# Kernel tuning notes

Hardware: AMD Instinct MI355X
Metric: run time of the kernel (lower is better)

Reference implementation:

```python
import jax, jax.numpy as jnp
import numpy as np

# Stickbreaking attention (IBM ModuleFormer style) as in the torch module:
#   logits = q @ k^T / sqrt(head_dim)  (causal)
#   z = sigmoid(logits), log_beta = logsigmoid(-logits), both causally masked
#   re_cum_log_beta = einsum('bhij,jk->bhik', log_beta, tril(ones(S,S)))
#     -> re[i,k] = sum_{k <= j <= i} log_beta[i, j]   (full tril incl. diagonal,
#        exactly as written in the source: cum_weight = torch.tril(torch.ones(L,L)))
#   weights = z * exp(re_cum_log_beta);  out = weights @ v
# Note: the torch code applies the causal mask by adding -inf; the only finite,
# NaN-free expression of that math (matching ModuleFormer's masked_fill) is to
# zero out masked entries of z and log_beta before the triangular matmul.

B, H, S, D = 2, 16, 1024, 64


def setup_inputs() -> dict:
    key = jax.random.key(0)
    kq, kk, kv = jax.random.split(key, 3)
    q = jax.random.normal(kq, (B, H, S, D), dtype=jnp.float32)
    k = jax.random.normal(kk, (B, H, S, D), dtype=jnp.float32)
    v = jax.random.normal(kv, (B, H, S, D), dtype=jnp.float32)
    return {"q": q, "k": k, "v": v}


def reference(q, k, v):
    head_dim = q.shape[-1]
    scaling = 1.0 / np.sqrt(head_dim).astype(np.float32)
    # [B,H,S,S] attention logits
    logits = jnp.einsum("bhqd,bhkd->bhqk", q, k) * scaling
    seq = logits.shape[-1]
    causal = jnp.tril(jnp.ones((seq, seq), dtype=logits.dtype))  # 1 where j<=i
    z = jax.nn.sigmoid(logits) * causal
    log_beta = jax.nn.log_sigmoid(-logits) * causal
    cum_weight = jnp.tril(jnp.ones((seq, seq), dtype=logits.dtype))
    # re[i,k] = sum_{j>=k} log_beta[i,j] (log_beta already 0 for j>i)
    re_cum_log_beta = jnp.einsum("bhij,jk->bhik", log_beta, cum_weight)
    weights = z * jnp.exp(re_cum_log_beta)
    return jnp.einsum("bhqk,bhkd->bhqd", weights, v)
```

## Files before the change

kernel.cpp:

```cpp
#include <hip/hip_runtime.h>
#include <hip/hip_bf16.h>
#include <math.h>


typedef __attribute__((ext_vector_type(8))) short short8;
typedef __attribute__((ext_vector_type(4))) short short4v;
typedef __attribute__((ext_vector_type(4))) float f32x4;

#define WPITCH 72
#define BLOB_SH 12288
#define NBLOB 512
#define VP 66

__device__ inline short bf16r(float x) {
    __hip_bfloat16 h = __float2bfloat16(x);
    return *(short*)&h;
}
__device__ inline float bf16f(short s) {
    union { unsigned u; float f; } c;
    c.u = ((unsigned)(unsigned short)s) << 16;
    return c.f;
}

__global__ __launch_bounds__(256) void stickbreak_prep(
    const float* __restrict__ Kg, const float* __restrict__ Vg,
    short* __restrict__ ws)
{
    __shared__ float Vlds[64 * VP];

    const int t = threadIdx.x;
    const int n = blockIdx.x;
    const float* kp = Kg + (size_t)n * 4096;
    const float* vp = Vg + (size_t)n * 4096;
    short* blob = ws + (size_t)n * BLOB_SH;

    const int lane = t & 63;
    const int l16 = lane & 15;
    const int q4 = lane >> 4;
    const int s0 = t >> 6;

    {
        const int row = t >> 2;
        const int cb = (t & 3) << 4;
        #pragma unroll
        for (int c = 0; c < 4; ++c) {
            const float4 f = *(const float4*)(vp + row * 64 + cb + 4 * c);
            *(float2*)&Vlds[row * VP + cb + 4 * c]     = make_float2(f.x, f.y);
            *(float2*)&Vlds[row * VP + cb + 4 * c + 2] = make_float2(f.z, f.w);
        }
    }

    #pragma unroll
    for (int w = 0; w < 2; ++w) {
        const int s  = s0 + 4 * w;
        const int nt = s >> 1;
        const int ks = s & 1;
        const float* src = kp + (16 * nt + l16) * 64 + 32 * ks + 8 * q4;
        const float4 f0 = *(const float4*)src;
        const float4 f1 = *(const float4*)(src + 4);
        float a[8] = {f0.x, f0.y, f0.z, f0.w, f1.x, f1.y, f1.z, f1.w};
        short8 h, l;
        #pragma unroll
        for (int e = 0; e < 8; ++e) {
            h[e] = bf16r(a[e]);
            l[e] = bf16r(a[e] - bf16f(h[e]));
        }
        *(short8*)&blob[s * 512 + lane * 8]        = h;
        *(short8*)&blob[4096 + s * 512 + lane * 8] = l;
    }

    __syncthreads();

    #pragma unroll
    for (int w = 0; w < 2; ++w) {
        const int s  = s0 + 4 * w;
        const int nt = s >> 1;
        const int ks = s & 1;
        const int d  = 16 * nt + l16;
        const int jb = 32 * ks + 8 * q4;
        short8 wv8;
        #pragma unroll
        for (int e = 0; e < 8; ++e) wv8[e] = bf16r(Vlds[(jb + e) * VP + d]);
        *(short8*)&blob[8192 + s * 512 + lane * 8] = wv8;
    }
}

__global__ __launch_bounds__(256, 4) void stickbreak_main(
    const float* __restrict__ Qg, const short* __restrict__ ws,
    float* __restrict__ part)
{
    __shared__ __align__(16) short Ws[64 * WPITCH];

    const int t = threadIdx.x;
    const int n = blockIdx.x;
    const int half = n >> 9;
    const int m = n & 511;
    const int bh = (m & 7) + 8 * (m >> 7);
    const int qr = (m >> 3) & 15;
    const int qt = (m >> 8) ? (15 - qr) : qr;
    const int nl = (qt + 1) >> 1;
    const int kstart = half ? (nl - 1) : qt;
    const int kend   = half ? 0 : nl;

    const size_t hbase = (size_t)bh * 1024 * 64;
    const float* qp = Qg + hbase + (size_t)qt * 64 * 64;
    const short* blobs = ws + (size_t)bh * 16 * BLOB_SH;
    const int g = bh * 16 + qt;
    float* opart = part + (size_t)g * 8192 + (half ? 4096 : 0);
    float* Cb = part + (size_t)NBLOB * 8192;

    const int lane = t & 63;
    const int wv   = t >> 6;
    const int l16  = lane & 15;
    const int q4   = lane >> 4;

    short8 qfh[2], qfl[2];
    {
        const float* qrow = qp + (16 * wv + l16) * 64;
        #pragma unroll
        for (int ks = 0; ks < 2; ++ks) {
            const int base = 32 * ks + 8 * q4;
            const float4 f0 = *(const float4*)(qrow + base);
            const float4 f1 = *(const float4*)(qrow + base + 4);
            float a[8] = {f0.x, f0.y, f0.z, f0.w, f1.x, f1.y, f1.z, f1.w};
            #pragma unroll
            for (int j = 0; j < 8; ++j) {
                const short hi = bf16r(a[j]);
                qfh[ks][j] = hi;
                qfl[ks][j] = bf16r(a[j] - bf16f(hi));
            }
        }
    }

    f32x4 Oacc[4];
    #pragma unroll
    for (int i = 0; i < 4; ++i) Oacc[i] = (f32x4){0.f, 0.f, 0.f, 0.f};
    float Crow = 0.f;

    for (int kt = kstart; kt >= kend; --kt) {
        const short* blob = blobs + (size_t)kt * BLOB_SH;

        f32x4 Sacc[4];
        #pragma unroll
        for (int i = 0; i < 4; ++i) Sacc[i] = (f32x4){0.f, 0.f, 0.f, 0.f};
        #pragma unroll
        for (int ks = 0; ks < 2; ++ks) {
            short8 kh[4], kl[4];
            #pragma unroll
            for (int nt = 0; nt < 4; ++nt) {
                const int s = nt * 2 + ks;
                kh[nt] = *(const short8*)&blob[s * 512 + lane * 8];
                kl[nt] = *(const short8*)&blob[4096 + s * 512 + lane * 8];
            }
            #pragma unroll
            for (int nt = 0; nt < 4; ++nt) {
                Sacc[nt] = __builtin_amdgcn_mfma_f32_16x16x32_bf16(kh[nt], qfh[ks], Sacc[nt], 0, 0, 0);
                Sacc[nt] = __builtin_amdgcn_mfma_f32_16x16x32_bf16(kl[nt], qfh[ks], Sacc[nt], 0, 0, 0);
                Sacc[nt] = __builtin_amdgcn_mfma_f32_16x16x32_bf16(kh[nt], qfl[ks], Sacc[nt], 0, 0, 0);
            }
        }

        short8 vb[8];
        #pragma unroll
        for (int s = 0; s < 8; ++s)
            vb[s] = *(const short8*)&blob[8192 + s * 512 + lane * 8];

        const bool diag = (half == 0) && (kt == qt);
        const int irow = 16 * wv + l16;
        float ex[4][4];
        float sR[4];
        #pragma unroll
        for (int nt = 0; nt < 4; ++nt) {
            float lbr[4], lv[4];
            #pragma unroll
            for (int reg = 0; reg < 4; ++reg) {
                float l = Sacc[nt][reg] * 0.125f;
                if (diag && (16 * nt + 4 * q4 + reg > irow)) l = -1e30f;
                const float e  = __expf(-fabsf(l));
                const float lb = -(fmaxf(l, 0.f) + __logf(1.f + e));
                lv[reg] = l; lbr[reg] = lb;
            }
            const float s3 = lbr[3];
            const float s2 = lbr[2] + s3;
            const float s1 = lbr[1] + s2;
            const float s0 = lbr[0] + s1;
            ex[nt][0] = lv[0] + lbr[0] + s0;
            ex[nt][1] = lv[1] + lbr[1] + s1;
            ex[nt][2] = lv[2] + lbr[2] + s2;
            ex[nt][3] = lv[3] + lbr[3] + s3;
            sR[nt] = s0;
        }
        float gq[4], Tn[4];
        #pragma unroll
        for (int nt = 0; nt < 4; ++nt) {
            float g2 = sR[nt];
            float u = __shfl_down(g2, 16, 64); if (q4 < 3) g2 += u;
            u = __shfl_down(g2, 32, 64);       if (q4 < 2) g2 += u;
            gq[nt] = g2;
            Tn[nt] = __shfl(g2, l16, 64);
        }
        const float TSa[4] = { Tn[1] + Tn[2] + Tn[3], Tn[2] + Tn[3], Tn[3], 0.f };
        #pragma unroll
        for (int nt = 0; nt < 4; ++nt) {
            const float cross = (gq[nt] - sR[nt]) + TSa[nt] + Crow;
            short4v w4;
            #pragma unroll
            for (int reg = 0; reg < 4; ++reg)
                w4[reg] = bf16r(__expf(ex[nt][reg] + cross));
            *(short4v*)&Ws[irow * WPITCH + 16 * nt + 4 * q4] = w4;
        }
        Crow += TSa[0] + Tn[0];

        #pragma unroll
        for (int ks = 0; ks < 2; ++ks) {
            const short8 wa = *(const short8*)&Ws[(16 * wv + l16) * WPITCH + 32 * ks + 8 * q4];
            #pragma unroll
            for (int dt = 0; dt < 4; ++dt) {
                Oacc[dt] = __builtin_amdgcn_mfma_f32_16x16x32_bf16(wa, vb[dt * 2 + ks], Oacc[dt], 0, 0, 0);
            }
        }
    }

    #pragma unroll
    for (int dt = 0; dt < 4; ++dt)
        #pragma unroll
        for (int r = 0; r < 4; ++r)
            opart[(16 * wv + 4 * q4 + r) * 64 + 16 * dt + l16] = Oacc[dt][r];
    if (half == 0 && q4 == 0)
        Cb[(size_t)g * 64 + 16 * wv + l16] = Crow;
}

__global__ __launch_bounds__(256) void stickbreak_merge(
    const float* __restrict__ part, float* __restrict__ out)
{
    const int g = blockIdx.x;
    const int t = threadIdx.x;
    const int i = t >> 2;
    const int c0 = (t & 3) << 4;
    const float* Ohi = part + (size_t)g * 8192 + i * 64 + c0;
    const float* Olo = Ohi + 4096;
    const float e = __expf(part[(size_t)NBLOB * 8192 + (size_t)g * 64 + i]);
    float* o = out + (size_t)g * 4096 + i * 64 + c0;
    #pragma unroll
    for (int c = 0; c < 4; ++c) {
        const float4 a = ((const float4*)Ohi)[c];
        const float4 b = ((const float4*)Olo)[c];
        float4 r;
        r.x = fmaf(e, b.x, a.x);
        r.y = fmaf(e, b.y, a.y);
        r.z = fmaf(e, b.z, a.z);
        r.w = fmaf(e, b.w, a.w);
        ((float4*)o)[c] = r;
    }
}

extern "C" void kernel_launch(void* const* d_in, const int* in_sizes, int n_in,
                              void* d_out, int out_size, void* d_ws, size_t ws_size,
                              hipStream_t stream) {
    const float* q = (const float*)d_in[0];
    const float* k = (const float*)d_in[1];
    const float* v = (const float*)d_in[2];
    float* out = (float*)d_out;
    short* ws = (short*)d_ws;
    float* part = (float*)(ws + (size_t)NBLOB * BLOB_SH);
    stickbreak_prep<<<dim3(512), dim3(256), 0, stream>>>(k, v, ws);
    stickbreak_main<<<dim3(1024), dim3(256), 0, stream>>>(q, ws, part);
    stickbreak_merge<<<dim3(512), dim3(256), 0, stream>>>(part, out);
}
```

Measured before the change: 107.6 us.

## Compute stickbreak weights as sigmoid products and prefetch next K tile

Replaces the log-domain suffix sums of logsigmoid terms with direct products of sigmoids. Each element now needs one exp and one reciprocal instead of exp, log, and a final exp, and only one exp and one log per tile carry the running log-sum. It also double-buffers the K hi/lo fragments in registers so the next tile's K loads overlap with the softmax-like math. The product form risks underflow precision loss, since it uses a clamp at 80, and the extra 64 live registers for K raise register pressure.

```diff
diff --git a/kernel.cpp b/kernel.cpp
--- a/kernel.cpp
+++ b/kernel.cpp
@@ -137,79 +137,98 @@
     for (int i = 0; i < 4; ++i) Oacc[i] = (f32x4){0.f, 0.f, 0.f, 0.f};
     float Crow = 0.f;
 
+    short8 kh[8], kl[8];
+    if (kstart >= kend) {
+        const short* b0 = blobs + (size_t)kstart * BLOB_SH;
+        #pragma unroll
+        for (int s = 0; s < 8; ++s) {
+            kh[s] = *(const short8*)&b0[s * 512 + lane * 8];
+            kl[s] = *(const short8*)&b0[4096 + s * 512 + lane * 8];
+        }
+    }
+
     for (int kt = kstart; kt >= kend; --kt) {
         const short* blob = blobs + (size_t)kt * BLOB_SH;
 
+        short8 vb[8];
+        #pragma unroll
+        for (int s = 0; s < 8; ++s)
+            vb[s] = *(const short8*)&blob[8192 + s * 512 + lane * 8];
+
         f32x4 Sacc[4];
         #pragma unroll
         for (int i = 0; i < 4; ++i) Sacc[i] = (f32x4){0.f, 0.f, 0.f, 0.f};
         #pragma unroll
         for (int ks = 0; ks < 2; ++ks) {
-            short8 kh[4], kl[4];
             #pragma unroll
             for (int nt = 0; nt < 4; ++nt) {
                 const int s = nt * 2 + ks;
-                kh[nt] = *(const short8*)&blob[s * 512 + lane * 8];
-                kl[nt] = *(const short8*)&blob[4096 + s * 512 + lane * 8];
-            }
-            #pragma unroll
-            for (int nt = 0; nt < 4; ++nt) {
-                Sacc[nt] = __builtin_amdgcn_mfma_f32_16x16x32_bf16(kh[nt], qfh[ks], Sacc[nt], 0, 0, 0);
-                Sacc[nt] = __builtin_amdgcn_mfma_f32_16x16x32_bf16(kl[nt], qfh[ks], Sacc[nt], 0, 0, 0);
-                Sacc[nt] = __builtin_amdgcn_mfma_f32_16x16x32_bf16(kh[nt], qfl[ks], Sacc[nt], 0, 0, 0);
-            }
-        }
-
-        short8 vb[8];
-        #pragma unroll
-        for (int s = 0; s < 8; ++s)
-            vb[s] = *(const short8*)&blob[8192 + s * 512 + lane * 8];
+                Sacc[nt] = __builtin_amdgcn_mfma_f32_16x16x32_bf16(kh[s], qfh[ks], Sacc[nt], 0, 0, 0);
+                Sacc[nt] = __builtin_amdgcn_mfma_f32_16x16x32_bf16(kl[s], qfh[ks], Sacc[nt], 0, 0, 0);
+                Sacc[nt] = __builtin_amdgcn_mfma_f32_16x16x32_bf16(kh[s], qfl[ks], Sacc[nt], 0, 0, 0);
+            }
+        }
+
+        if (kt > kend) {
+            const short* nb = blobs + (size_t)(kt - 1) * BLOB_SH;
+            #pragma unroll
+            for (int s = 0; s < 8; ++s) {
+                kh[s] = *(const short8*)&nb[s * 512 + lane * 8];
+                kl[s] = *(const short8*)&nb[4096 + s * 512 + lane * 8];
+            }
+        }
 
         const bool diag = (half == 0) && (kt == qt);
         const int irow = 16 * wv + l16;
-        float ex[4][4];
-        float sR[4];
+        const float E = __expf(Crow);
+        float zw[4][4];
+        float R[4];
         #pragma unroll
         for (int nt = 0; nt < 4; ++nt) {
-            float lbr[4], lv[4];
+            float sg[4], zz[4];
             #pragma unroll
             for (int reg = 0; reg < 4; ++reg) {
                 float l = Sacc[nt][reg] * 0.125f;
                 if (diag && (16 * nt + 4 * q4 + reg > irow)) l = -1e30f;
-                const float e  = __expf(-fabsf(l));
-                const float lb = -(fmaxf(l, 0.f) + __logf(1.f + e));
-                lv[reg] = l; lbr[reg] = lb;
-            }
-            const float s3 = lbr[3];
-            const float s2 = lbr[2] + s3;
-            const float s1 = lbr[1] + s2;
-            const float s0 = lbr[0] + s1;
-            ex[nt][0] = lv[0] + lbr[0] + s0;
-            ex[nt][1] = lv[1] + lbr[1] + s1;
-            ex[nt][2] = lv[2] + lbr[2] + s2;
-            ex[nt][3] = lv[3] + lbr[3] + s3;
-            sR[nt] = s0;
-        }
-        float gq[4], Tn[4];
+                l = fminf(l, 80.f);
+                const float el = __expf(l);
+                const float s  = __builtin_amdgcn_rcpf(1.f + el);
+                sg[reg] = s;
+                zz[reg] = el * s;
+            }
+            const float p3 = sg[3];
+            const float p2 = sg[2] * p3;
+            const float p1 = sg[1] * p2;
+            const float p0 = sg[0] * p1;
+            zw[nt][0] = zz[0] * p0;
+            zw[nt][1] = zz[1] * p1;
+            zw[nt][2] = zz[2] * p2;
+            zw[nt][3] = zz[3] * p3;
+            R[nt] = p0;
+        }
+        float exq[4], Tn[4];
         #pragma unroll
         for (int nt = 0; nt < 4; ++nt) {
-            float g2 = sR[nt];
-            float u = __shfl_down(g2, 16, 64); if (q4 < 3) g2 += u;
-            u = __shfl_down(g2, 32, 64);       if (q4 < 2) g2 += u;
-            gq[nt] = g2;
-            Tn[nt] = __shfl(g2, l16, 64);
-        }
-        const float TSa[4] = { Tn[1] + Tn[2] + Tn[3], Tn[2] + Tn[3], Tn[3], 0.f };
+            float gq = R[nt];
+            float u = __shfl_down(gq, 16, 64); if (q4 < 3) gq *= u;
+            u = __shfl_down(gq, 32, 64);       if (q4 < 2) gq *= u;
+            float ex_ = __shfl_down(gq, 16, 64);
+            exq[nt] = (q4 < 3) ? ex_ : 1.f;
+            Tn[nt]  = __shfl(gq, l16, 64);
+        }
+        const float TSa1 = Tn[2] * Tn[3];
+        const float TSa0 = Tn[1] * TSa1;
+        const float TSa[4] = { TSa0, TSa1, Tn[3], 1.f };
         #pragma unroll
         for (int nt = 0; nt < 4; ++nt) {
-            const float cross = (gq[nt] - sR[nt]) + TSa[nt] + Crow;
+            const float mfac = exq[nt] * TSa[nt] * E;
             short4v w4;
             #pragma unroll
             for (int reg = 0; reg < 4; ++reg)
-                w4[reg] = bf16r(__expf(ex[nt][reg] + cross));
+                w4[reg] = bf16r(zw[nt][reg] * mfac);
             *(short4v*)&Ws[irow * WPITCH + 16 * nt + 4 * q4] = w4;
         }
-        Crow += TSa[0] + Tn[0];
+        Crow += __logf(Tn[0] * TSa0);
 
         #pragma unroll
         for (int ks = 0; ks < 2; ++ks) {
```

New measurement: 175.1 us. 62.7% more time.
